# Kernel optimization log

Hardware: AMD Instinct MI355X
Metric: run time of the kernel (lower is better)

The kernel has to match this reference:

```python
import jax, jax.numpy as jnp
import numpy as np

SEP = 2            # sep_token_id
B, S, H = 8, 4096, 768
MAX_SENT = 64      # = labels.size(1) in the original
STD = 0.02         # initializer_range


def setup_inputs() -> dict:
    key = jax.random.key(0)
    ks = jax.random.split(key, 6)
    hidden = jax.random.normal(ks[0], (B, S, H), jnp.float32)
    ids = jax.random.randint(ks[1], (B, S), 5, 30000, dtype=jnp.int64)
    # plant a sep every 64 tokens -> 64 seps, 64 non-empty sentences per row
    ids = ids.at[:, 63::64].set(SEP)
    W1 = jax.random.normal(ks[2], (H, 4096), jnp.float32) * STD
    b1 = jnp.zeros((4096,), jnp.float32)
    W2 = jax.random.normal(ks[3], (4096, 256), jnp.float32) * STD
    b2 = jnp.zeros((256,), jnp.float32)
    W3 = jax.random.normal(ks[4], (256, 2), jnp.float32) * STD
    b3 = jnp.zeros((2,), jnp.float32)
    return dict(hidden=hidden, input_ids=ids, W1=W1, b1=b1, W2=W2, b2=b2, W3=W3, b3=b3)


def _pool_row(h, ids):
    # h: [S, H], ids: [S] -> per-sentence means [MAX_SENT, H]
    sep = (ids == SEP)
    sep_i = sep.astype(jnp.int32)
    # exclusive cumsum: segment id = number of seps strictly before position t
    seg = jnp.cumsum(sep_i) - sep_i
    pos = jnp.arange(S)
    first_sep = jnp.argmax(sep)
    n_sep = sep_i.sum()
    # original includes the FIRST sep in sentence 0 but excludes later seps,
    # and excludes the last token of the trailing (post-last-sep) segment
    weight = jnp.where(sep, pos == first_sep, True)
    weight = weight & ~((pos == S - 1) & (seg == n_sep) & (n_sep > 0))
    # truncate to max_sentences: overflow segments land in a dump bucket
    seg_c = jnp.minimum(seg, MAX_SENT)
    hw = jnp.where(weight[:, None], h, 0.0)
    sums = jax.ops.segment_sum(hw, seg_c, num_segments=MAX_SENT + 1)[:MAX_SENT]
    cnts = jax.ops.segment_sum(weight.astype(h.dtype), seg_c, num_segments=MAX_SENT + 1)[:MAX_SENT]
    # empty (padding) segments -> zeros, matching the original zero-padding
    return jnp.where(cnts[:, None] > 0, sums / jnp.maximum(cnts, 1.0)[:, None], 0.0)


def reference(hidden, input_ids, W1, b1, W2, b2, W3, b3):
    # [B, MAX_SENT, H] per-sentence mean representations
    sent = jax.vmap(_pool_row)(hidden, input_ids)
    # classifier head (dropout = identity in eval); GELU is exact (torch nn.GELU default)
    x = jax.nn.gelu(jnp.einsum('bmh,hf->bmf', sent, W1) + b1, approximate=False)
    x = jax.nn.gelu(jnp.einsum('bmf,fg->bmg', x, W2) + b2, approximate=False)
    logits = jnp.einsum('bmg,gc->bmc', x, W3) + b3  # [B, MAX_SENT, 2]
    return logits
```

## Files before the change

kernel.cpp:

```cpp
#include <hip/hip_runtime.h>
#include <hip/hip_bf16.h>

#define SEP_ID 2
#define S_LEN  4096
#define HID    768
#define MAXS   64

using short8  = __attribute__((ext_vector_type(8))) short;
using floatx4 = __attribute__((ext_vector_type(4))) float;

__device__ __forceinline__ float gelu_exact(float x) {
    return 0.5f * x * (1.0f + erff(x * 0.70710678118654752f));
}

__global__ __launch_bounds__(256) void stage1_kernel(const int* __restrict__ ids,
                                                     const float* __restrict__ hidden,
                                                     const float* __restrict__ W1,
                                                     const float* __restrict__ W2,
                                                     __hip_bfloat16* __restrict__ W1T,
                                                     __hip_bfloat16* __restrict__ W2T,
                                                     __hip_bfloat16* __restrict__ sentb) {
    __shared__ __align__(16) char smem[16640];
    const int blk = blockIdx.x;
    const int t = threadIdx.x;

    if (blk < 512) {
        int* sep_pos = (int*)smem;
        int* wtot    = sep_pos + 4096;
        const int sidx = blk;
        const int b = sidx >> 6, m = sidx & 63;
        const int* row = ids + (size_t)b * S_LEN;
        const int lane = t & 63, w = t >> 6;

        int local[16]; int c = 0;
        const int base = t * 16;
        #pragma unroll
        for (int q = 0; q < 4; ++q) {
            int4 v = ((const int4*)row)[t * 4 + q];
            if (v.x == SEP_ID) local[c++] = base + q * 4 + 0;
            if (v.y == SEP_ID) local[c++] = base + q * 4 + 1;
            if (v.z == SEP_ID) local[c++] = base + q * 4 + 2;
            if (v.w == SEP_ID) local[c++] = base + q * 4 + 3;
        }
        int scan = c;
        #pragma unroll
        for (int off = 1; off < 64; off <<= 1) {
            int n = __shfl_up(scan, off);
            if (lane >= off) scan += n;
        }
        if (lane == 63) wtot[w] = scan;
        __syncthreads();
        int wbase = 0;
        for (int i = 0; i < w; ++i) wbase += wtot[i];
        const int o = wbase + scan - c;
        for (int i = 0; i < c; ++i) sep_pos[o + i] = local[i];
        __syncthreads();
        const int n_sep = wtot[0] + wtot[1] + wtot[2] + wtot[3];

        int start = 0, cnt = 0;
        if (n_sep == 0) {
            if (m == 0) { start = 0; cnt = S_LEN; }
        } else if (m < n_sep) {
            if (m == 0) { start = 0; cnt = sep_pos[0] + 1; }
            else { start = sep_pos[m - 1] + 1; cnt = sep_pos[m] - sep_pos[m - 1] - 1; }
        } else if (m == n_sep) {
            start = sep_pos[n_sep - 1] + 1;
            cnt = (S_LEN - 1) - start;
            if (cnt < 0) cnt = 0;
        }

        if (t < 192) {
            const float4* bp = (const float4*)(hidden + ((size_t)b * S_LEN + start) * HID);
            float ax = 0.f, ay = 0.f, az = 0.f, aw = 0.f;
            int i = 0;
            for (; i + 8 <= cnt; i += 8) {
                float4 v[8];
                #pragma unroll
                for (int j = 0; j < 8; ++j) v[j] = bp[(size_t)(i + j) * 192 + t];
                #pragma unroll
                for (int j = 0; j < 8; ++j) { ax += v[j].x; ay += v[j].y; az += v[j].z; aw += v[j].w; }
            }
            for (; i < cnt; ++i) {
                float4 v = bp[(size_t)i * 192 + t];
                ax += v.x; ay += v.y; az += v.z; aw += v.w;
            }
            const float inv = (cnt > 0) ? 1.0f / (float)cnt : 0.0f;
            __hip_bfloat16 h0 = __float2bfloat16(ax * inv);
            __hip_bfloat16 h1 = __float2bfloat16(ay * inv);
            __hip_bfloat16 h2 = __float2bfloat16(az * inv);
            __hip_bfloat16 h3 = __float2bfloat16(aw * inv);
            ushort4 pk;
            pk.x = *(unsigned short*)&h0; pk.y = *(unsigned short*)&h1;
            pk.z = *(unsigned short*)&h2; pk.w = *(unsigned short*)&h3;
            *(ushort4*)(sentb + (size_t)sidx * HID + t * 4) = pk;
        }
    } else {
        float* tile = (float*)smem;
        const int id0 = blk - 512;
        const float* in; __hip_bfloat16* outw; int K, N, n0, k0;
        if (id0 < 3072) { in = W1; outw = W1T; K = 768;  N = 4096;
                          n0 = (id0 & 127) * 32; k0 = (id0 >> 7) * 32; }
        else { const int id = id0 - 3072;
               in = W2; outw = W2T; K = 4096; N = 256;
               n0 = (id & 7) * 32; k0 = (id >> 3) * 32; }
        const int c = t & 31;
        const int r = t >> 5;
        #pragma unroll
        for (int i = 0; i < 32; i += 8)
            tile[(r + i) * 33 + c] = in[(size_t)(k0 + r + i) * N + n0 + c];
        __syncthreads();
        #pragma unroll
        for (int i = 0; i < 32; i += 8)
            outw[(size_t)(n0 + r + i) * K + k0 + c] = __float2bfloat16(tile[c * 33 + r + i]);
    }
}

__global__ __launch_bounds__(256) void gemm1_kernel(const __hip_bfloat16* __restrict__ A,
                                                    const __hip_bfloat16* __restrict__ BT,
                                                    const float* __restrict__ bias,
                                                    __hip_bfloat16* __restrict__ out) {
    const int n0 = blockIdx.x * 64;
    const int m0 = blockIdx.y * 64;
    const int t = threadIdx.x;
    const int w = t >> 6, l = t & 63;
    const int wm = (w >> 1) * 32;
    const int wn = (w & 1) * 32;

    __shared__ __hip_bfloat16 Al[64][136];
    __shared__ __hip_bfloat16 Bl[64][136];

    floatx4 acc[2][2] = {};

    const int r  = t >> 2;
    const int ch = (t & 3) * 32;
    const __hip_bfloat16* Ag = A  + (size_t)(m0 + r) * 768 + ch;
    const __hip_bfloat16* Bg = BT + (size_t)(n0 + r) * 768 + ch;

    const int lr = l & 15;
    const int kq = (l >> 4) * 8;

    for (int k0 = 0; k0 < 768; k0 += 128) {
        short8 av[4], bv[4];
        #pragma unroll
        for (int q = 0; q < 4; ++q) {
            av[q] = *(const short8*)(Ag + k0 + q * 8);
            bv[q] = *(const short8*)(Bg + k0 + q * 8);
        }
        __syncthreads();
        #pragma unroll
        for (int q = 0; q < 4; ++q) {
            *(short8*)(&Al[r][ch + q * 8]) = av[q];
            *(short8*)(&Bl[r][ch + q * 8]) = bv[q];
        }
        __syncthreads();

        #pragma unroll
        for (int ks = 0; ks < 128; ks += 32) {
            short8 a0 = *(const short8*)(&Al[wm + lr][ks + kq]);
            short8 a1 = *(const short8*)(&Al[wm + 16 + lr][ks + kq]);
            short8 b0 = *(const short8*)(&Bl[wn + lr][ks + kq]);
            short8 b1 = *(const short8*)(&Bl[wn + 16 + lr][ks + kq]);
            acc[0][0] = __builtin_amdgcn_mfma_f32_16x16x32_bf16(a0, b0, acc[0][0], 0, 0, 0);
            acc[0][1] = __builtin_amdgcn_mfma_f32_16x16x32_bf16(a0, b1, acc[0][1], 0, 0, 0);
            acc[1][0] = __builtin_amdgcn_mfma_f32_16x16x32_bf16(a1, b0, acc[1][0], 0, 0, 0);
            acc[1][1] = __builtin_amdgcn_mfma_f32_16x16x32_bf16(a1, b1, acc[1][1], 0, 0, 0);
        }
    }

    __syncthreads();
    __hip_bfloat16* E = &Al[0][0];
    #pragma unroll
    for (int i = 0; i < 2; ++i) {
        #pragma unroll
        for (int j = 0; j < 2; ++j) {
            const int cl = wn + j * 16 + lr;
            const float bv = bias[n0 + cl];
            #pragma unroll
            for (int rg = 0; rg < 4; ++rg) {
                const int rl = wm + i * 16 + (l >> 4) * 4 + rg;
                float x = acc[i][j][rg] + bv;
                E[rl * 72 + cl] = __float2bfloat16(gelu_exact(x));
            }
        }
    }
    __syncthreads();
    {
        const int rr  = t >> 2;
        const int seg = (t & 3) * 16;
        short8 v0 = *(const short8*)(&E[rr * 72 + seg]);
        short8 v1 = *(const short8*)(&E[rr * 72 + seg + 8]);
        __hip_bfloat16* op = out + (size_t)(m0 + rr) * 4096 + n0 + seg;
        *(short8*)(op)     = v0;
        *(short8*)(op + 8) = v1;
    }
}

__global__ __launch_bounds__(256) void gemm2_kernel(const __hip_bfloat16* __restrict__ A,
                                                    const __hip_bfloat16* __restrict__ BT,
                                                    float* __restrict__ part) {
    const int n0 = blockIdx.x * 64;
    const int m0 = blockIdx.y * 64;
    const int s  = blockIdx.z;
    const int kb = s * 512;
    const int t = threadIdx.x;
    const int w = t >> 6, l = t & 63;
    const int wm = (w >> 1) * 32;
    const int wn = (w & 1) * 32;

    __shared__ __hip_bfloat16 Al[64][136];
    __shared__ __hip_bfloat16 Bl[64][136];

    floatx4 acc[2][2] = {};

    const int r  = t >> 2;
    const int ch = (t & 3) * 32;
    const __hip_bfloat16* Ag = A  + (size_t)(m0 + r) * 4096 + kb + ch;
    const __hip_bfloat16* Bg = BT + (size_t)(n0 + r) * 4096 + kb + ch;

    const int lr = l & 15;
    const int kq = (l >> 4) * 8;

    for (int k0 = 0; k0 < 512; k0 += 128) {
        short8 av[4], bv[4];
        #pragma unroll
        for (int q = 0; q < 4; ++q) {
            av[q] = *(const short8*)(Ag + k0 + q * 8);
            bv[q] = *(const short8*)(Bg + k0 + q * 8);
        }
        __syncthreads();
        #pragma unroll
        for (int q = 0; q < 4; ++q) {
            *(short8*)(&Al[r][ch + q * 8]) = av[q];
            *(short8*)(&Bl[r][ch + q * 8]) = bv[q];
        }
        __syncthreads();

        #pragma unroll
        for (int ks = 0; ks < 128; ks += 32) {
            short8 a0 = *(const short8*)(&Al[wm + lr][ks + kq]);
            short8 a1 = *(const short8*)(&Al[wm + 16 + lr][ks + kq]);
            short8 b0 = *(const short8*)(&Bl[wn + lr][ks + kq]);
            short8 b1 = *(const short8*)(&Bl[wn + 16 + lr][ks + kq]);
            acc[0][0] = __builtin_amdgcn_mfma_f32_16x16x32_bf16(a0, b0, acc[0][0], 0, 0, 0);
            acc[0][1] = __builtin_amdgcn_mfma_f32_16x16x32_bf16(a0, b1, acc[0][1], 0, 0, 0);
            acc[1][0] = __builtin_amdgcn_mfma_f32_16x16x32_bf16(a1, b0, acc[1][0], 0, 0, 0);
            acc[1][1] = __builtin_amdgcn_mfma_f32_16x16x32_bf16(a1, b1, acc[1][1], 0, 0, 0);
        }
    }

    float* po = part + (size_t)s * 512 * 256;
    #pragma unroll
    for (int i = 0; i < 2; ++i) {
        #pragma unroll
        for (int j = 0; j < 2; ++j) {
            const int col  = n0 + wn + j * 16 + lr;
            const int rowb = m0 + wm + i * 16 + (l >> 4) * 4;
            #pragma unroll
            for (int rg = 0; rg < 4; ++rg)
                po[(size_t)(rowb + rg) * 256 + col] = acc[i][j][rg];
        }
    }
}

__global__ __launch_bounds__(256) void rh_kernel(const float* __restrict__ part,
                                                 const float* __restrict__ b2,
                                                 const float* __restrict__ W3,
                                                 const float* __restrict__ b3,
                                                 float* __restrict__ out) {
    const int row = blockIdx.x;
    const int c = threadIdx.x;
    const int w = c >> 6, l = c & 63;

    float s = 0.f;
    #pragma unroll
    for (int k = 0; k < 8; ++k)
        s += part[((size_t)k * 512 + row) * 256 + c];
    const float x = gelu_exact(s + b2[c]);
    float y0 = x * W3[c * 2 + 0];
    float y1 = x * W3[c * 2 + 1];
    #pragma unroll
    for (int off = 32; off; off >>= 1) {
        y0 += __shfl_down(y0, off);
        y1 += __shfl_down(y1, off);
    }
    __shared__ float r0[4], r1[4];
    if (l == 0) { r0[w] = y0; r1[w] = y1; }
    __syncthreads();
    if (c == 0) out[row * 2 + 0] = r0[0] + r0[1] + r0[2] + r0[3] + b3[0];
    if (c == 1) out[row * 2 + 1] = r1[0] + r1[1] + r1[2] + r1[3] + b3[1];
}

extern "C" void kernel_launch(void* const* d_in, const int* in_sizes, int n_in,
                              void* d_out, int out_size, void* d_ws, size_t ws_size,
                              hipStream_t stream) {
    const float* hidden = (const float*)d_in[0];
    const int*   ids    = (const int*)d_in[1];
    const float* W1     = (const float*)d_in[2];
    const float* b1     = (const float*)d_in[3];
    const float* W2     = (const float*)d_in[4];
    const float* b2     = (const float*)d_in[5];
    const float* W3     = (const float*)d_in[6];
    const float* b3     = (const float*)d_in[7];
    float* out = (float*)d_out;

    char* ws = (char*)d_ws;
    __hip_bfloat16* sentb  = (__hip_bfloat16*)(ws + 0);
    __hip_bfloat16* W1T    = (__hip_bfloat16*)(ws + 786432);
    __hip_bfloat16* W2T    = (__hip_bfloat16*)(ws + 7077888);
    __hip_bfloat16* x1     = (__hip_bfloat16*)(ws + 9175040);
    float* part            = (float*)(ws + 13369344);

    stage1_kernel<<<4608, 256, 0, stream>>>(ids, hidden, W1, W2, W1T, W2T, sentb);
    gemm1_kernel<<<dim3(64, 8), 256, 0, stream>>>(sentb, W1T, b1, x1);
    gemm2_kernel<<<dim3(4, 8, 8), 256, 0, stream>>>(x1, W2T, part);
    rh_kernel<<<512, 256, 0, stream>>>(part, b2, W3, b3, out);
}
```

Before: 195.1 us.

## Fuse weight bf16 conversion into GEMM loads and split-K reduction into gemm2

Stops pre-transposing W1 and W2 to bf16 in a separate stage. The GEMMs now read the fp32 weights directly, pack pairs of k-rows to bf16 and write them transposed into shared memory. The split-K partial sums are accumulated with atomicAdd into a zeroed fp32 buffer, and the last-arriving block per row tile (counted with an atomic) applies GELU and the final 256x2 projection, which removes rh_kernel. This drops a full weight transpose pass and one kernel launch, at the cost of fp32 weight reads inside the GEMMs, float atomics and a nondeterministic summation order.

Result: slower. 243.3 us (+24.7%).

```diff
diff --git a/kernel.cpp b/kernel.cpp
--- a/kernel.cpp
+++ b/kernel.cpp
@@ -13,114 +13,103 @@
     return 0.5f * x * (1.0f + erff(x * 0.70710678118654752f));
 }
 
+__device__ __forceinline__ unsigned pack_bf16x2(float lo, float hi) {
+    __hip_bfloat16 a = __float2bfloat16(lo);
+    __hip_bfloat16 b = __float2bfloat16(hi);
+    return ((unsigned)*(unsigned short*)&b << 16) | (unsigned)*(unsigned short*)&a;
+}
+
 __global__ __launch_bounds__(256) void stage1_kernel(const int* __restrict__ ids,
                                                      const float* __restrict__ hidden,
-                                                     const float* __restrict__ W1,
-                                                     const float* __restrict__ W2,
-                                                     __hip_bfloat16* __restrict__ W1T,
-                                                     __hip_bfloat16* __restrict__ W2T,
-                                                     __hip_bfloat16* __restrict__ sentb) {
-    __shared__ __align__(16) char smem[16640];
+                                                     __hip_bfloat16* __restrict__ sentb,
+                                                     float* __restrict__ x2,
+                                                     int* __restrict__ cnt) {
+    __shared__ __align__(16) int smem[4100];
     const int blk = blockIdx.x;
     const int t = threadIdx.x;
 
-    if (blk < 512) {
-        int* sep_pos = (int*)smem;
-        int* wtot    = sep_pos + 4096;
-        const int sidx = blk;
-        const int b = sidx >> 6, m = sidx & 63;
-        const int* row = ids + (size_t)b * S_LEN;
-        const int lane = t & 63, w = t >> 6;
-
-        int local[16]; int c = 0;
-        const int base = t * 16;
-        #pragma unroll
-        for (int q = 0; q < 4; ++q) {
-            int4 v = ((const int4*)row)[t * 4 + q];
-            if (v.x == SEP_ID) local[c++] = base + q * 4 + 0;
-            if (v.y == SEP_ID) local[c++] = base + q * 4 + 1;
-            if (v.z == SEP_ID) local[c++] = base + q * 4 + 2;
-            if (v.w == SEP_ID) local[c++] = base + q * 4 + 3;
-        }
-        int scan = c;
-        #pragma unroll
-        for (int off = 1; off < 64; off <<= 1) {
-            int n = __shfl_up(scan, off);
-            if (lane >= off) scan += n;
-        }
-        if (lane == 63) wtot[w] = scan;
-        __syncthreads();
-        int wbase = 0;
-        for (int i = 0; i < w; ++i) wbase += wtot[i];
-        const int o = wbase + scan - c;
-        for (int i = 0; i < c; ++i) sep_pos[o + i] = local[i];
-        __syncthreads();
-        const int n_sep = wtot[0] + wtot[1] + wtot[2] + wtot[3];
-
-        int start = 0, cnt = 0;
-        if (n_sep == 0) {
-            if (m == 0) { start = 0; cnt = S_LEN; }
-        } else if (m < n_sep) {
-            if (m == 0) { start = 0; cnt = sep_pos[0] + 1; }
-            else { start = sep_pos[m - 1] + 1; cnt = sep_pos[m] - sep_pos[m - 1] - 1; }
-        } else if (m == n_sep) {
-            start = sep_pos[n_sep - 1] + 1;
-            cnt = (S_LEN - 1) - start;
-            if (cnt < 0) cnt = 0;
-        }
-
-        if (t < 192) {
-            const float4* bp = (const float4*)(hidden + ((size_t)b * S_LEN + start) * HID);
-            float ax = 0.f, ay = 0.f, az = 0.f, aw = 0.f;
-            int i = 0;
-            for (; i + 8 <= cnt; i += 8) {
-                float4 v[8];
-                #pragma unroll
-                for (int j = 0; j < 8; ++j) v[j] = bp[(size_t)(i + j) * 192 + t];
-                #pragma unroll
-                for (int j = 0; j < 8; ++j) { ax += v[j].x; ay += v[j].y; az += v[j].z; aw += v[j].w; }
-            }
-            for (; i < cnt; ++i) {
-                float4 v = bp[(size_t)i * 192 + t];
-                ax += v.x; ay += v.y; az += v.z; aw += v.w;
-            }
-            const float inv = (cnt > 0) ? 1.0f / (float)cnt : 0.0f;
-            __hip_bfloat16 h0 = __float2bfloat16(ax * inv);
-            __hip_bfloat16 h1 = __float2bfloat16(ay * inv);
-            __hip_bfloat16 h2 = __float2bfloat16(az * inv);
-            __hip_bfloat16 h3 = __float2bfloat16(aw * inv);
-            ushort4 pk;
-            pk.x = *(unsigned short*)&h0; pk.y = *(unsigned short*)&h1;
-            pk.z = *(unsigned short*)&h2; pk.w = *(unsigned short*)&h3;
-            *(ushort4*)(sentb + (size_t)sidx * HID + t * 4) = pk;
-        }
-    } else {
-        float* tile = (float*)smem;
-        const int id0 = blk - 512;
-        const float* in; __hip_bfloat16* outw; int K, N, n0, k0;
-        if (id0 < 3072) { in = W1; outw = W1T; K = 768;  N = 4096;
-                          n0 = (id0 & 127) * 32; k0 = (id0 >> 7) * 32; }
-        else { const int id = id0 - 3072;
-               in = W2; outw = W2T; K = 4096; N = 256;
-               n0 = (id & 7) * 32; k0 = (id >> 3) * 32; }
-        const int c = t & 31;
-        const int r = t >> 5;
-        #pragma unroll
-        for (int i = 0; i < 32; i += 8)
-            tile[(r + i) * 33 + c] = in[(size_t)(k0 + r + i) * N + n0 + c];
-        __syncthreads();
-        #pragma unroll
-        for (int i = 0; i < 32; i += 8)
-            outw[(size_t)(n0 + r + i) * K + k0 + c] = __float2bfloat16(tile[c * 33 + r + i]);
+    if (blk >= 512) {
+        float4* p = (float4*)x2 + (size_t)(blk - 512) * 2048 + t;
+        float4 z = {0.f, 0.f, 0.f, 0.f};
+        #pragma unroll
+        for (int i = 0; i < 8; ++i) p[i * 256] = z;
+        if (blk == 512 && t < 16) cnt[t] = 0;
+        return;
+    }
+
+    int* sep_pos = smem;
+    int* wtot    = sep_pos + 4096;
+    const int sidx = blk;
+    const int b = sidx >> 6, m = sidx & 63;
+    const int* row = ids + (size_t)b * S_LEN;
+    const int lane = t & 63, w = t >> 6;
+
+    int local[16]; int c = 0;
+    const int base = t * 16;
+    #pragma unroll
+    for (int q = 0; q < 4; ++q) {
+        int4 v = ((const int4*)row)[t * 4 + q];
+        if (v.x == SEP_ID) local[c++] = base + q * 4 + 0;
+        if (v.y == SEP_ID) local[c++] = base + q * 4 + 1;
+        if (v.z == SEP_ID) local[c++] = base + q * 4 + 2;
+        if (v.w == SEP_ID) local[c++] = base + q * 4 + 3;
+    }
+    int scan = c;
+    #pragma unroll
+    for (int off = 1; off < 64; off <<= 1) {
+        int n = __shfl_up(scan, off);
+        if (lane >= off) scan += n;
+    }
+    if (lane == 63) wtot[w] = scan;
+    __syncthreads();
+    int wbase = 0;
+    for (int i = 0; i < w; ++i) wbase += wtot[i];
+    const int o = wbase + scan - c;
+    for (int i = 0; i < c; ++i) sep_pos[o + i] = local[i];
+    __syncthreads();
+    const int n_sep = wtot[0] + wtot[1] + wtot[2] + wtot[3];
+
+    int start = 0, cntok = 0;
+    if (n_sep == 0) {
+        if (m == 0) { start = 0; cntok = S_LEN; }
+    } else if (m < n_sep) {
+        if (m == 0) { start = 0; cntok = sep_pos[0] + 1; }
+        else { start = sep_pos[m - 1] + 1; cntok = sep_pos[m] - sep_pos[m - 1] - 1; }
+    } else if (m == n_sep) {
+        start = sep_pos[n_sep - 1] + 1;
+        cntok = (S_LEN - 1) - start;
+        if (cntok < 0) cntok = 0;
+    }
+
+    if (t < 192) {
+        const float4* bp = (const float4*)(hidden + ((size_t)b * S_LEN + start) * HID);
+        float ax = 0.f, ay = 0.f, az = 0.f, aw = 0.f;
+        int i = 0;
+        for (; i + 8 <= cntok; i += 8) {
+            float4 v[8];
+            #pragma unroll
+            for (int j = 0; j < 8; ++j) v[j] = bp[(size_t)(i + j) * 192 + t];
+            #pragma unroll
+            for (int j = 0; j < 8; ++j) { ax += v[j].x; ay += v[j].y; az += v[j].z; aw += v[j].w; }
+        }
+        for (; i < cntok; ++i) {
+            float4 v = bp[(size_t)i * 192 + t];
+            ax += v.x; ay += v.y; az += v.z; aw += v.w;
+        }
+        const float inv = (cntok > 0) ? 1.0f / (float)cntok : 0.0f;
+        unsigned p0 = pack_bf16x2(ax * inv, ay * inv);
+        unsigned p1 = pack_bf16x2(az * inv, aw * inv);
+        uint2 pk = {p0, p1};
+        *(uint2*)(sentb + (size_t)sidx * HID + t * 4) = pk;
     }
 }
 
 __global__ __launch_bounds__(256) void gemm1_kernel(const __hip_bfloat16* __restrict__ A,
-                                                    const __hip_bfloat16* __restrict__ BT,
+                                                    const float* __restrict__ W1,
                                                     const float* __restrict__ bias,
                                                     __hip_bfloat16* __restrict__ out) {
-    const int n0 = blockIdx.x * 64;
-    const int m0 = blockIdx.y * 64;
+    const int m0 = blockIdx.x * 64;
+    const int n0 = blockIdx.y * 64;
     const int t = threadIdx.x;
     const int w = t >> 6, l = t & 63;
     const int wm = (w >> 1) * 32;
@@ -133,25 +122,36 @@
 
     const int r  = t >> 2;
     const int ch = (t & 3) * 32;
-    const __hip_bfloat16* Ag = A  + (size_t)(m0 + r) * 768 + ch;
-    const __hip_bfloat16* Bg = BT + (size_t)(n0 + r) * 768 + ch;
+    const __hip_bfloat16* Ag = A + (size_t)(m0 + r) * 768 + ch;
+
+    const int kp   = t >> 2;
+    const int nseg = (t & 3) * 16;
 
     const int lr = l & 15;
     const int kq = (l >> 4) * 8;
 
     for (int k0 = 0; k0 < 768; k0 += 128) {
-        short8 av[4], bv[4];
+        short8 av[4];
+        #pragma unroll
+        for (int q = 0; q < 4; ++q) av[q] = *(const short8*)(Ag + k0 + q * 8);
+
+        const float* bp0 = W1 + (size_t)(k0 + 2 * kp) * 4096 + n0 + nseg;
+        const float* bp1 = bp0 + 4096;
+        float fa[16], fb[16];
         #pragma unroll
         for (int q = 0; q < 4; ++q) {
-            av[q] = *(const short8*)(Ag + k0 + q * 8);
-            bv[q] = *(const short8*)(Bg + k0 + q * 8);
-        }
+            float4 v0 = ((const float4*)bp0)[q];
+            float4 v1 = ((const float4*)bp1)[q];
+            fa[q*4+0] = v0.x; fa[q*4+1] = v0.y; fa[q*4+2] = v0.z; fa[q*4+3] = v0.w;
+            fb[q*4+0] = v1.x; fb[q*4+1] = v1.y; fb[q*4+2] = v1.z; fb[q*4+3] = v1.w;
+        }
+
         __syncthreads();
         #pragma unroll
-        for (int q = 0; q < 4; ++q) {
-            *(short8*)(&Al[r][ch + q * 8]) = av[q];
-            *(short8*)(&Bl[r][ch + q * 8]) = bv[q];
-        }
+        for (int q = 0; q < 4; ++q) *(short8*)(&Al[r][ch + q * 8]) = av[q];
+        #pragma unroll
+        for (int j = 0; j < 16; ++j)
+            *(unsigned*)(&Bl[nseg + j][2 * kp]) = pack_bf16x2(fa[j], fb[j]);
         __syncthreads();
 
         #pragma unroll
@@ -196,10 +196,15 @@
 }
 
 __global__ __launch_bounds__(256) void gemm2_kernel(const __hip_bfloat16* __restrict__ A,
-                                                    const __hip_bfloat16* __restrict__ BT,
-                                                    float* __restrict__ part) {
-    const int n0 = blockIdx.x * 64;
-    const int m0 = blockIdx.y * 64;
+                                                    const float* __restrict__ W2,
+                                                    const float* __restrict__ b2,
+                                                    const float* __restrict__ W3,
+                                                    const float* __restrict__ b3,
+                                                    float* __restrict__ x2,
+                                                    int* __restrict__ cnt,
+                                                    float* __restrict__ out) {
+    const int m0 = blockIdx.x * 64;
+    const int n0 = blockIdx.y * 64;
     const int s  = blockIdx.z;
     const int kb = s * 512;
     const int t = threadIdx.x;
@@ -209,30 +214,42 @@
 
     __shared__ __hip_bfloat16 Al[64][136];
     __shared__ __hip_bfloat16 Bl[64][136];
+    __shared__ int lastflag;
 
     floatx4 acc[2][2] = {};
 
     const int r  = t >> 2;
     const int ch = (t & 3) * 32;
-    const __hip_bfloat16* Ag = A  + (size_t)(m0 + r) * 4096 + kb + ch;
-    const __hip_bfloat16* Bg = BT + (size_t)(n0 + r) * 4096 + kb + ch;
+    const __hip_bfloat16* Ag = A + (size_t)(m0 + r) * 4096 + kb + ch;
+
+    const int kp   = t >> 2;
+    const int nseg = (t & 3) * 16;
 
     const int lr = l & 15;
     const int kq = (l >> 4) * 8;
 
     for (int k0 = 0; k0 < 512; k0 += 128) {
-        short8 av[4], bv[4];
+        short8 av[4];
+        #pragma unroll
+        for (int q = 0; q < 4; ++q) av[q] = *(const short8*)(Ag + k0 + q * 8);
+
+        const float* bp0 = W2 + (size_t)(kb + k0 + 2 * kp) * 256 + n0 + nseg;
+        const float* bp1 = bp0 + 256;
+        float fa[16], fb[16];
         #pragma unroll
         for (int q = 0; q < 4; ++q) {
-            av[q] = *(const short8*)(Ag + k0 + q * 8);
-            bv[q] = *(const short8*)(Bg + k0 + q * 8);
-        }
+            float4 v0 = ((const float4*)bp0)[q];
+            float4 v1 = ((const float4*)bp1)[q];
+            fa[q*4+0] = v0.x; fa[q*4+1] = v0.y; fa[q*4+2] = v0.z; fa[q*4+3] = v0.w;
+            fb[q*4+0] = v1.x; fb[q*4+1] = v1.y; fb[q*4+2] = v1.z; fb[q*4+3] = v1.w;
+        }
+
         __syncthreads();
         #pragma unroll
-        for (int q = 0; q < 4; ++q) {
-            *(short8*)(&Al[r][ch + q * 8]) = av[q];
-            *(short8*)(&Bl[r][ch + q * 8]) = bv[q];
-        }
+        for (int q = 0; q < 4; ++q) *(short8*)(&Al[r][ch + q * 8]) = av[q];
+        #pragma unroll
+        for (int j = 0; j < 16; ++j)
+            *(unsigned*)(&Bl[nseg + j][2 * kp]) = pack_bf16x2(fa[j], fb[j]);
         __syncthreads();
 
         #pragma unroll
@@ -248,7 +265,6 @@
         }
     }
 
-    float* po = part + (size_t)s * 512 * 256;
     #pragma unroll
     for (int i = 0; i < 2; ++i) {
         #pragma unroll
@@ -257,37 +273,41 @@
             const int rowb = m0 + wm + i * 16 + (l >> 4) * 4;
             #pragma unroll
             for (int rg = 0; rg < 4; ++rg)
-                po[(size_t)(rowb + rg) * 256 + col] = acc[i][j][rg];
-        }
-    }
-}
-
-__global__ __launch_bounds__(256) void rh_kernel(const float* __restrict__ part,
-                                                 const float* __restrict__ b2,
-                                                 const float* __restrict__ W3,
-                                                 const float* __restrict__ b3,
-                                                 float* __restrict__ out) {
-    const int row = blockIdx.x;
-    const int c = threadIdx.x;
-    const int w = c >> 6, l = c & 63;
-
-    float s = 0.f;
-    #pragma unroll
-    for (int k = 0; k < 8; ++k)
-        s += part[((size_t)k * 512 + row) * 256 + c];
-    const float x = gelu_exact(s + b2[c]);
-    float y0 = x * W3[c * 2 + 0];
-    float y1 = x * W3[c * 2 + 1];
-    #pragma unroll
-    for (int off = 32; off; off >>= 1) {
-        y0 += __shfl_down(y0, off);
-        y1 += __shfl_down(y1, off);
-    }
-    __shared__ float r0[4], r1[4];
-    if (l == 0) { r0[w] = y0; r1[w] = y1; }
-    __syncthreads();
-    if (c == 0) out[row * 2 + 0] = r0[0] + r0[1] + r0[2] + r0[3] + b3[0];
-    if (c == 1) out[row * 2 + 1] = r1[0] + r1[1] + r1[2] + r1[3] + b3[1];
+                atomicAdd(&x2[(size_t)(rowb + rg) * 256 + col], acc[i][j][rg]);
+        }
+    }
+
+    __threadfence();
+    __syncthreads();
+    if (t == 0) {
+        int old = atomicAdd(&cnt[blockIdx.x], 1);
+        lastflag = (old == 31);
+    }
+    __syncthreads();
+    if (!lastflag) return;
+    __threadfence();
+
+    for (int it = 0; it < 16; ++it) {
+        const int row = m0 + it * 4 + w;
+        float y0 = 0.f, y1 = 0.f;
+        #pragma unroll
+        for (int q = 0; q < 4; ++q) {
+            const int col = l + 64 * q;
+            const float v = x2[(size_t)row * 256 + col];
+            const float x = gelu_exact(v + b2[col]);
+            y0 += x * W3[col * 2 + 0];
+            y1 += x * W3[col * 2 + 1];
+        }
+        #pragma unroll
+        for (int off = 32; off; off >>= 1) {
+            y0 += __shfl_down(y0, off);
+            y1 += __shfl_down(y1, off);
+        }
+        if (l == 0) {
+            out[row * 2 + 0] = y0 + b3[0];
+            out[row * 2 + 1] = y1 + b3[1];
+        }
+    }
 }
 
 extern "C" void kernel_launch(void* const* d_in, const int* in_sizes, int n_in,
@@ -304,14 +324,12 @@
     float* out = (float*)d_out;
 
     char* ws = (char*)d_ws;
-    __hip_bfloat16* sentb  = (__hip_bfloat16*)(ws + 0);
-    __hip_bfloat16* W1T    = (__hip_bfloat16*)(ws + 786432);
-    __hip_bfloat16* W2T    = (__hip_bfloat16*)(ws + 7077888);
-    __hip_bfloat16* x1     = (__hip_bfloat16*)(ws + 9175040);
-    float* part            = (float*)(ws + 13369344);
-
-    stage1_kernel<<<4608, 256, 0, stream>>>(ids, hidden, W1, W2, W1T, W2T, sentb);
-    gemm1_kernel<<<dim3(64, 8), 256, 0, stream>>>(sentb, W1T, b1, x1);
-    gemm2_kernel<<<dim3(4, 8, 8), 256, 0, stream>>>(x1, W2T, part);
-    rh_kernel<<<512, 256, 0, stream>>>(part, b2, W3, b3, out);
-}
+    __hip_bfloat16* sentb = (__hip_bfloat16*)(ws + 0);
+    __hip_bfloat16* x1    = (__hip_bfloat16*)(ws + 786432);
+    float* x2             = (float*)(ws + 4980736);
+    int*   cnt            = (int*)(ws + 5505024);
+
+    stage1_kernel<<<528, 256, 0, stream>>>(ids, hidden, sentb, x2, cnt);
+    gemm1_kernel<<<dim3(8, 64), 256, 0, stream>>>(sentb, W1, b1, x1);
+    gemm2_kernel<<<dim3(8, 4, 8), 256, 0, stream>>>(x1, W2, b2, W3, b3, x2, cnt, out);
+}
```
